# Optimization experiments

Hardware: AMD Instinct MI355X
Metric: run time of the kernel (lower is better)

The kernel has to match this reference:

```python
import jax, jax.numpy as jnp
import numpy as np

COLB = 16            # COL_BLOCK_WIDTH
IN_W = 1024          # input_width; zero_inputs=0 so input_locations = arange(IN_W)
OUT_W = 512          # output_width
DEPTH = 8            # network_depth
IN_L = 4             # butterfly_in_depth
OUT_L = 4            # butterfly_out_depth
ACT = 8              # activations_per_block
BLOCKS = 64          # blocks_per_layer -> num_inputs = 1024 per module
CURV = 1.0
GROW = BLOCKS * ACT  # 512 new rows per module
TOTAL = IN_W + DEPTH * GROW  # 5120
BATCH = 4096


def setup_inputs() -> dict:
    key = jax.random.key(0)
    k1, k2, k3 = jax.random.split(key, 3)
    input_data = jax.random.normal(k1, (IN_W, BATCH), dtype=jnp.float32)
    scales = jnp.full((IN_W,), 0.05, dtype=jnp.float32)
    # angles uniform in (-pi, pi), shape [depth, in_layers+out_layers, num_inputs/2]
    angles = (jax.random.uniform(k2, (DEPTH, IN_L + OUT_L, BLOCKS * COLB // 2)) * 2.0 - 1.0) * np.pi
    angles = angles.astype(jnp.float32)
    biases = jax.random.normal(k3, (DEPTH, GROW), dtype=jnp.float32) * 0.05
    # per-module indices_in = randperm(total_width_so_far)[:num_inputs]
    rng = np.random.RandomState(0)
    tw = IN_W
    idxs = []
    for _ in range(DEPTH):
        idxs.append(rng.permutation(tw)[: BLOCKS * COLB].astype(np.int32))
        tw += GROW
    indices_in = jnp.asarray(np.stack(idxs))  # [depth, 1024]
    return {"input_data": input_data, "scales": scales, "angles": angles,
            "biases": biases, "indices_in": indices_in}


def _rotate(x, ang, stride):
    # x: [W, B]; pair row i (with (i//stride)%2==0) with row i+stride inside 16-blocks
    W, B = x.shape
    xr = x.reshape(W // (2 * stride), 2, stride, B)
    a = ang.reshape(W // (2 * stride), stride)[:, :, None]
    c, s = jnp.cos(a), jnp.sin(a)
    lo, hi = xr[:, 0], xr[:, 1]              # [W/2s, s, B]
    nlo = c * lo + s * hi
    nhi = -s * lo + c * hi
    return jnp.stack([nlo, nhi], axis=1).reshape(W, B)


def _butterfly_module(data, ang, bias, idx, idx_out):
    W = BLOCKS * COLB
    x = data[idx]                             # gather [1024, B]
    for l in range(IN_L):
        x = _rotate(x, ang[l], 2 ** (l % 4))
    xb = x.reshape(BLOCKS, COLB, -1)
    pre = xb[:, :ACT, :] + bias.reshape(BLOCKS, ACT)[:, :, None]
    # curvature (smoothed-ReLU) activation
    act = 0.5 * (pre + jnp.sqrt(pre * pre + CURV * CURV))
    xb = xb.at[:, :ACT, :].set(act)
    x = xb.reshape(W, -1)
    for l in range(OUT_L):
        x = _rotate(x, ang[IN_L + l], 2 ** ((IN_L + l) % 4))
    data = data.at[idx].set(x)                # scatter working set back
    data = data.at[idx_out: idx_out + GROW].set(act.reshape(GROW, -1))
    return data


def reference(input_data, scales, angles, biases, indices_in):
    B = input_data.shape[1]
    data = jnp.zeros((TOTAL, B), dtype=input_data.dtype)
    data = data.at[:IN_W].set(scales[:, None] * input_data)
    for i in range(DEPTH):
        data = _butterfly_module(data, angles[i], biases[i], indices_in[i], IN_W + GROW * i)
    return data[TOTAL - OUT_W:]
```

## Files before the change

### kernel.cpp

```cpp
#include <hip/hip_runtime.h>
#include <math.h>

#define N_INW     1024
#define N_DEPTH   8
#define N_GROW    512
#define N_BATCH   4096
#define N_THREADS 64
#define N_LAYERS  64

typedef __attribute__((ext_vector_type(2))) float F2;
typedef decltype(__builtin_amdgcn_cvt_pkrtz(0.f, 0.f)) H2;

__global__ void precompute_kernel(const float* __restrict__ angles,
                                  const int*   __restrict__ indices,
                                  _Float16* __restrict__ csh,
                                  int*   __restrict__ addrs) {
    int i = blockIdx.x * blockDim.x + threadIdx.x;
    if (i < N_LAYERS * 512) {
        int g = i >> 9, p = i & 511, blk = p >> 3, j = p & 7;
        float a = angles[i];
        _Float16* base = csh + g * 1024 + blk * 16;
        base[j]     = (_Float16)cosf(a);
        base[8 + j] = (_Float16)sinf(a);
    }
    if (i < N_DEPTH * N_INW) {
        int v = indices[i];
        addrs[i] = (v + (v >> 4)) << 2;
    }
}

#define ADDR(r) ((((r) + ((r) >> 4))) << 2)

#define LD2(A) ({ H2 _h = *(const H2*)(L + (A));                               \
                  F2 _v; _v.x = (float)_h.x; _v.y = (float)_h.y; _v; })
#define ST2(A, V) do { F2 _w = (V);                                            \
    *(H2*)(L + (A)) = __builtin_amdgcn_cvt_pkrtz(_w.x, _w.y); } while (0)

#define PKU(x, y) __builtin_bit_cast(unsigned int,                             \
                      __builtin_amdgcn_cvt_pkrtz((x), (y)))

#define UNPK(Q, FA, FB) do {                                                   \
    H2 _h0 = __builtin_bit_cast(H2, (Q).x), _h1 = __builtin_bit_cast(H2, (Q).y),\
       _h2 = __builtin_bit_cast(H2, (Q).z), _h3 = __builtin_bit_cast(H2, (Q).w);\
    FA.x = (float)_h0.x; FA.y = (float)_h0.y; FA.z = (float)_h1.x;             \
    FA.w = (float)_h1.y; FB.x = (float)_h2.x; FB.y = (float)_h2.y;             \
    FB.z = (float)_h3.x; FB.w = (float)_h3.y; } while (0)

#define DECL_SET(P)                                                            \
    uint4 P##c0, P##s0, P##c1, P##s1, P##c2, P##s2, P##c3, P##s3,              \
          P##c4, P##s4, P##c5, P##s5, P##c6, P##s6, P##c7, P##s7;              \
    int4  P##i0, P##i1, P##i2, P##i3;                                          \
    float4 P##bA, P##bB;

#define SYN1(P, K, ANB) do {                                                   \
    const float4* _p = (const float4*)((ANB) + (K)*512 + (blk << 3));          \
    float4 _u = _p[0], _v = _p[1];                                             \
    float _c0,_c1,_c2,_c3,_c4,_c5,_c6,_c7,_t0,_t1,_t2,_t3,_t4,_t5,_t6,_t7;     \
    __sincosf(_u.x,&_t0,&_c0); __sincosf(_u.y,&_t1,&_c1);                      \
    __sincosf(_u.z,&_t2,&_c2); __sincosf(_u.w,&_t3,&_c3);                      \
    __sincosf(_v.x,&_t4,&_c4); __sincosf(_v.y,&_t5,&_c5);                      \
    __sincosf(_v.z,&_t6,&_c6); __sincosf(_v.w,&_t7,&_c7);                      \
    P##c##K = make_uint4(PKU(_c0,_c1),PKU(_c2,_c3),PKU(_c4,_c5),PKU(_c6,_c7)); \
    P##s##K = make_uint4(PKU(_t0,_t1),PKU(_t2,_t3),PKU(_t4,_t5),PKU(_t6,_t7)); \
  } while (0)

#define LOADCS1(P, K, CSN, ANB) do { if (USE_TABLE) {                          \
    const char* _b = (CSN) + (blk << 5) + (K)*2048;                            \
    P##c##K = *(const uint4*)(_b); P##s##K = *(const uint4*)(_b + 16);         \
  } else { SYN1(P, K, ANB); } } while (0)

#define LOADCS8(P, CSN, ANB) do {                                              \
    LOADCS1(P,0,CSN,ANB); LOADCS1(P,1,CSN,ANB); LOADCS1(P,2,CSN,ANB);          \
    LOADCS1(P,3,CSN,ANB); LOADCS1(P,4,CSN,ANB); LOADCS1(P,5,CSN,ANB);          \
    LOADCS1(P,6,CSN,ANB); LOADCS1(P,7,CSN,ANB); } while (0)
#define LOADCS4(P, CSN, ANB) do {                                              \
    LOADCS1(P,0,CSN,ANB); LOADCS1(P,1,CSN,ANB); LOADCS1(P,2,CSN,ANB);          \
    LOADCS1(P,3,CSN,ANB); } while (0)

#define TR(v) (((v) + ((v) >> 4)) << 2)
#define LOAD_AB(P, ATN, INB, BIN) do { if (USE_TABLE) {                        \
    const int4* _ip = (const int4*)((ATN) + (blk << 4));                       \
    P##i0=_ip[0]; P##i1=_ip[1]; P##i2=_ip[2]; P##i3=_ip[3];                    \
  } else {                                                                     \
    const int4* _ip = (const int4*)((INB) + (blk << 4));                       \
    int4 _v0=_ip[0], _v1=_ip[1], _v2=_ip[2], _v3=_ip[3];                       \
    P##i0.x=TR(_v0.x); P##i0.y=TR(_v0.y); P##i0.z=TR(_v0.z); P##i0.w=TR(_v0.w);\
    P##i1.x=TR(_v1.x); P##i1.y=TR(_v1.y); P##i1.z=TR(_v1.z); P##i1.w=TR(_v1.w);\
    P##i2.x=TR(_v2.x); P##i2.y=TR(_v2.y); P##i2.z=TR(_v2.z); P##i2.w=TR(_v2.w);\
    P##i3.x=TR(_v3.x); P##i3.y=TR(_v3.y); P##i3.z=TR(_v3.z); P##i3.w=TR(_v3.w);\
  }                                                                            \
  const float4* _bp = (const float4*)((BIN) + (blk << 3));                     \
  P##bA = _bp[0]; P##bB = _bp[1]; } while (0)

#define ROTP(LO, HI, CC, SS) do { F2 _l = LO, _h = HI;                         \
    LO = CC * _l + SS * _h; HI = CC * _h - SS * _l; } while (0)

#define ROTS1(CA,CB,SA,SB) do {                                                \
    ROTP(x0,x1,CA.x,SA.x);  ROTP(x2,x3,CA.y,SA.y);                             \
    ROTP(x4,x5,CA.z,SA.z);  ROTP(x6,x7,CA.w,SA.w);                             \
    ROTP(x8,x9,CB.x,SB.x);  ROTP(x10,x11,CB.y,SB.y);                           \
    ROTP(x12,x13,CB.z,SB.z);ROTP(x14,x15,CB.w,SB.w); } while (0)
#define ROTS2(CA,CB,SA,SB) do {                                                \
    ROTP(x0,x2,CA.x,SA.x);  ROTP(x1,x3,CA.y,SA.y);                             \
    ROTP(x4,x6,CA.z,SA.z);  ROTP(x5,x7,CA.w,SA.w);                             \
    ROTP(x8,x10,CB.x,SB.x); ROTP(x9,x11,CB.y,SB.y);                            \
    ROTP(x12,x14,CB.z,SB.z);ROTP(x13,x15,CB.w,SB.w); } while (0)
#define ROTS4(CA,CB,SA,SB) do {                                                \
    ROTP(x0,x4,CA.x,SA.x);  ROTP(x1,x5,CA.y,SA.y);                             \
    ROTP(x2,x6,CA.z,SA.z);  ROTP(x3,x7,CA.w,SA.w);                             \
    ROTP(x8,x12,CB.x,SB.x); ROTP(x9,x13,CB.y,SB.y);                            \
    ROTP(x10,x14,CB.z,SB.z);ROTP(x11,x15,CB.w,SB.w); } while (0)
#define ROTS8(CA,CB,SA,SB) do {                                                \
    ROTP(x0,x8,CA.x,SA.x);  ROTP(x1,x9,CA.y,SA.y);                             \
    ROTP(x2,x10,CA.z,SA.z); ROTP(x3,x11,CA.w,SA.w);                            \
    ROTP(x4,x12,CB.x,SB.x); ROTP(x5,x13,CB.y,SB.y);                            \
    ROTP(x6,x14,CB.z,SB.z); ROTP(x7,x15,CB.w,SB.w); } while (0)

#define ROTL(P, K, ROTM) do { float4 _CA,_CB,_SA,_SB;                          \
    UNPK(P##c##K, _CA, _CB); UNPK(P##s##K, _SA, _SB);                          \
    ROTM(_CA,_CB,_SA,_SB); } while (0)

#define ACT1(X, BB) do { F2 _p = (X) + (BB);                                   \
    F2 _t = _p * _p + 1.0f;                                                    \
    F2 _r; _r.x = __builtin_amdgcn_sqrtf(_t.x);                                \
    _r.y = __builtin_amdgcn_sqrtf(_t.y);                                       \
    X = 0.5f * (_p + _r); } while (0)

#define FENCE() __builtin_amdgcn_sched_barrier(0)

#define PROC_MOD(P, N, CSN, ANN, ATN, INB, BIN, M, FULL) do {                  \
  const int a0=P##i0.x, a1=P##i0.y, a2=P##i0.z, a3=P##i0.w,                    \
            a4=P##i1.x, a5=P##i1.y, a6=P##i1.z, a7=P##i1.w,                    \
            a8=P##i2.x, a9=P##i2.y, a10=P##i2.z, a11=P##i2.w,                  \
            a12=P##i3.x, a13=P##i3.y, a14=P##i3.z, a15=P##i3.w;                \
  F2 x0=LD2(a0), x1=LD2(a1), x2=LD2(a2), x3=LD2(a3),                           \
     x4=LD2(a4), x5=LD2(a5), x6=LD2(a6), x7=LD2(a7),                           \
     x8=LD2(a8), x9=LD2(a9), x10=LD2(a10), x11=LD2(a11),                       \
     x12=LD2(a12), x13=LD2(a13), x14=LD2(a14), x15=LD2(a15);                   \
  if (FULL) { LOADCS8(N, CSN, ANN); } else { LOADCS4(N, CSN, ANN); }           \
  FENCE();                                                                     \
                     \
  ROTL(P,0,ROTS1); ROTL(P,1,ROTS2); ROTL(P,2,ROTS4); ROTL(P,3,ROTS8);          \
  ACT1(x0,P##bA.x); ACT1(x1,P##bA.y); ACT1(x2,P##bA.z); ACT1(x3,P##bA.w);      \
  ACT1(x4,P##bB.x); ACT1(x5,P##bB.y); ACT1(x6,P##bB.z); ACT1(x7,P##bB.w);      \
  const int _ab = ADDR(N_INW + (M)*N_GROW + (blk << 3));                       \
  ST2(_ab+ 0,x0); ST2(_ab+ 4,x1); ST2(_ab+ 8,x2); ST2(_ab+12,x3);              \
  ST2(_ab+16,x4); ST2(_ab+20,x5); ST2(_ab+24,x6); ST2(_ab+28,x7);              \
  LOAD_AB(N, ATN, INB, BIN);                                                   \
  FENCE();                                                                     \
  ROTL(P,4,ROTS1); ROTL(P,5,ROTS2); ROTL(P,6,ROTS4); ROTL(P,7,ROTS8);          \
  ST2(a0,x0);  ST2(a1,x1);  ST2(a2,x2);  ST2(a3,x3);                           \
  ST2(a4,x4);  ST2(a5,x5);  ST2(a6,x6);  ST2(a7,x7);                           \
  ST2(a8,x8);  ST2(a9,x9);  ST2(a10,x10); ST2(a11,x11);                        \
  ST2(a12,x12); ST2(a13,x13); ST2(a14,x14); ST2(a15,x15);                      \
} while (0)

template <bool USE_TABLE>
__global__ __launch_bounds__(N_THREADS, 2)
void butterfly_fused_kernel(const float* __restrict__ input,
                            const float* __restrict__ scales,
                            const float* __restrict__ biases,
                            const int*   __restrict__ indices,
                            const char*  __restrict__ cs_tab,
                            const int*   __restrict__ addr_tab,
                            const float* __restrict__ angles,
                            float* __restrict__ out) {
    extern __shared__ float ldsbuf[];
    char* L = (char*)ldsbuf;
    const int blk = threadIdx.x;
    const int b   = blockIdx.x;
    const int cg  = (((b & 7) * 256) + (b >> 3)) * 2;

    DECL_SET(A) DECL_SET(B)

    LOADCS8(A, cs_tab, angles);
    LOAD_AB(A, addr_tab, indices, biases);

#pragma unroll
    for (int k = 0; k < 16; ++k) {
        const int r = (k << 6) + blk;
        F2 v = *(const F2*)(input + (size_t)r * N_BATCH + cg);
        ST2(ADDR(r), scales[r] * v);
    }

    const char*  csn = cs_tab + 16384;
    const float* ann = angles + 4096;
    const int*   atn = addr_tab + N_INW;
    const int*   inb = indices + N_INW;
    const float* bin = biases + N_GROW;

#pragma unroll 1
    for (int t = 0; t < 3; ++t) {
        const int m = 2 * t;
        PROC_MOD(A, B, csn, ann, atn, inb, bin, m, 1);
        csn += 16384; ann += 4096; atn += N_INW; inb += N_INW; bin += N_GROW;
        PROC_MOD(B, A, csn, ann, atn, inb, bin, m + 1, 1);
        csn += 16384; ann += 4096; atn += N_INW; inb += N_INW; bin += N_GROW;
    }
    PROC_MOD(A, B, csn, ann, atn, inb, bin, 6, 0);

    {
        const int a0=Bi0.x, a1=Bi0.y, a2=Bi0.z, a3=Bi0.w,
                  a4=Bi1.x, a5=Bi1.y, a6=Bi1.z, a7=Bi1.w;
        F2 x0=LD2(a0), x1=LD2(a1), x2=LD2(a2), x3=LD2(a3),
           x4=LD2(a4), x5=LD2(a5), x6=LD2(a6), x7=LD2(a7);
        F2 x8=LD2(Bi2.x), x9=LD2(Bi2.y), x10=LD2(Bi2.z), x11=LD2(Bi2.w),
           x12=LD2(Bi3.x), x13=LD2(Bi3.y), x14=LD2(Bi3.z), x15=LD2(Bi3.w);
        FENCE();
        ROTL(B,0,ROTS1); ROTL(B,1,ROTS2); ROTL(B,2,ROTS4); ROTL(B,3,ROTS8);
        ACT1(x0,BbA.x); ACT1(x1,BbA.y); ACT1(x2,BbA.z); ACT1(x3,BbA.w);
        ACT1(x4,BbB.x); ACT1(x5,BbB.y); ACT1(x6,BbB.z); ACT1(x7,BbB.w);
        *(F2*)(out + (size_t)((blk<<3)+0)*N_BATCH + cg) = x0;
        *(F2*)(out + (size_t)((blk<<3)+1)*N_BATCH + cg) = x1;
        *(F2*)(out + (size_t)((blk<<3)+2)*N_BATCH + cg) = x2;
        *(F2*)(out + (size_t)((blk<<3)+3)*N_BATCH + cg) = x3;
        *(F2*)(out + (size_t)((blk<<3)+4)*N_BATCH + cg) = x4;
        *(F2*)(out + (size_t)((blk<<3)+5)*N_BATCH + cg) = x5;
        *(F2*)(out + (size_t)((blk<<3)+6)*N_BATCH + cg) = x6;
        *(F2*)(out + (size_t)((blk<<3)+7)*N_BATCH + cg) = x7;
    }
}

extern "C" void kernel_launch(void* const* d_in, const int* in_sizes, int n_in,
                              void* d_out, int out_size, void* d_ws, size_t ws_size,
                              hipStream_t stream) {
    const float* input   = (const float*)d_in[0];
    const float* scales  = (const float*)d_in[1];
    const float* angles  = (const float*)d_in[2];
    const float* biases  = (const float*)d_in[3];
    const int*   indices = (const int*)d_in[4];
    float* out = (float*)d_out;

    const size_t cs_bytes  = (size_t)N_LAYERS * 2048;
    const size_t adr_bytes = (size_t)N_DEPTH * N_INW * sizeof(int);
    const size_t lds_bytes = (size_t)4608 * 4 + 288 * 4;
    const int grid = N_BATCH / 2;

    if (ws_size >= cs_bytes + adr_bytes) {
        _Float16* csh = (_Float16*)d_ws;
        int* addrs = (int*)((char*)d_ws + cs_bytes);
        precompute_kernel<<<(N_LAYERS * 512 + 255) / 256, 256, 0, stream>>>(
            angles, indices, csh, addrs);
        butterfly_fused_kernel<true><<<grid, N_THREADS, lds_bytes, stream>>>(
            input, scales, biases, indices, (const char*)csh, addrs, angles, out);
    } else {
        butterfly_fused_kernel<false><<<grid, N_THREADS, lds_bytes, stream>>>(
            input, scales, biases, indices, nullptr, nullptr, angles, out);
    }
}
```

Baseline: 100.5 us.

## Run butterfly rotations in packed fp16 and give each block two column-pair slabs

Rotations now run directly on packed half2 values, using broadcast cos/sin halves, instead of unpacking to fp32 and repacking. This removes many conversion instructions per layer, though the rotation arithmetic is now done in fp16 rather than fp32. The activation still runs in fp32 on each element. Blocks grow to 128 threads, where two wavefronts each own their own LDS slab and column pair, and the grid is halved. This amortises per-block setup but may reduce occupancy because each block needs more LDS.

```diff
diff --git a/kernel.cpp b/kernel.cpp
--- a/kernel.cpp
+++ b/kernel.cpp
@@ -5,11 +5,12 @@
 #define N_DEPTH   8
 #define N_GROW    512
 #define N_BATCH   4096
-#define N_THREADS 64
+#define N_THREADS 128
 #define N_LAYERS  64
-
-typedef __attribute__((ext_vector_type(2))) float F2;
-typedef decltype(__builtin_amdgcn_cvt_pkrtz(0.f, 0.f)) H2;
+#define SLAB_B    19584
+
+typedef __attribute__((ext_vector_type(2))) float    F2;
+typedef __attribute__((ext_vector_type(2))) _Float16 h2;
 
 __global__ void precompute_kernel(const float* __restrict__ angles,
                                   const int*   __restrict__ indices,
@@ -31,20 +32,20 @@
 
 #define ADDR(r) ((((r) + ((r) >> 4))) << 2)
 
-#define LD2(A) ({ H2 _h = *(const H2*)(L + (A));                               \
-                  F2 _v; _v.x = (float)_h.x; _v.y = (float)_h.y; _v; })
-#define ST2(A, V) do { F2 _w = (V);                                            \
-    *(H2*)(L + (A)) = __builtin_amdgcn_cvt_pkrtz(_w.x, _w.y); } while (0)
+#define LDH(A)    __builtin_bit_cast(h2, *(const unsigned*)(L + (A)))
+#define STH(A, V) do { *(unsigned*)(L + (A)) =                                 \
+                       __builtin_bit_cast(unsigned, (V)); } while (0)
 
 #define PKU(x, y) __builtin_bit_cast(unsigned int,                             \
                       __builtin_amdgcn_cvt_pkrtz((x), (y)))
 
-#define UNPK(Q, FA, FB) do {                                                   \
-    H2 _h0 = __builtin_bit_cast(H2, (Q).x), _h1 = __builtin_bit_cast(H2, (Q).y),\
-       _h2 = __builtin_bit_cast(H2, (Q).z), _h3 = __builtin_bit_cast(H2, (Q).w);\
-    FA.x = (float)_h0.x; FA.y = (float)_h0.y; FA.z = (float)_h1.x;             \
-    FA.w = (float)_h1.y; FB.x = (float)_h2.x; FB.y = (float)_h2.y;             \
-    FB.z = (float)_h3.x; FB.w = (float)_h3.y; } while (0)
+#define BCL(U) ({ h2 _t = __builtin_bit_cast(h2, (unsigned)(U));               \
+                  h2 _r; _r.x = _t.x; _r.y = _t.x; _r; })
+#define BCH(U) ({ h2 _t = __builtin_bit_cast(h2, (unsigned)(U));               \
+                  h2 _r; _r.x = _t.y; _r.y = _t.y; _r; })
+
+#define ROTPH(LO, HI, CC, SS) do { h2 _l = LO, _h = HI, _c = CC, _s = SS;      \
+    LO = _c * _l + _s * _h; HI = _c * _h - _s * _l; } while (0)
 
 #define DECL_SET(P)                                                            \
     uint4 P##c0, P##s0, P##c1, P##s1, P##c2, P##s2, P##c3, P##s3,              \
@@ -92,39 +93,38 @@
   const float4* _bp = (const float4*)((BIN) + (blk << 3));                     \
   P##bA = _bp[0]; P##bB = _bp[1]; } while (0)
 
-#define ROTP(LO, HI, CC, SS) do { F2 _l = LO, _h = HI;                         \
-    LO = CC * _l + SS * _h; HI = CC * _h - SS * _l; } while (0)
-
-#define ROTS1(CA,CB,SA,SB) do {                                                \
-    ROTP(x0,x1,CA.x,SA.x);  ROTP(x2,x3,CA.y,SA.y);                             \
-    ROTP(x4,x5,CA.z,SA.z);  ROTP(x6,x7,CA.w,SA.w);                             \
-    ROTP(x8,x9,CB.x,SB.x);  ROTP(x10,x11,CB.y,SB.y);                           \
-    ROTP(x12,x13,CB.z,SB.z);ROTP(x14,x15,CB.w,SB.w); } while (0)
-#define ROTS2(CA,CB,SA,SB) do {                                                \
-    ROTP(x0,x2,CA.x,SA.x);  ROTP(x1,x3,CA.y,SA.y);                             \
-    ROTP(x4,x6,CA.z,SA.z);  ROTP(x5,x7,CA.w,SA.w);                             \
-    ROTP(x8,x10,CB.x,SB.x); ROTP(x9,x11,CB.y,SB.y);                            \
-    ROTP(x12,x14,CB.z,SB.z);ROTP(x13,x15,CB.w,SB.w); } while (0)
-#define ROTS4(CA,CB,SA,SB) do {                                                \
-    ROTP(x0,x4,CA.x,SA.x);  ROTP(x1,x5,CA.y,SA.y);                             \
-    ROTP(x2,x6,CA.z,SA.z);  ROTP(x3,x7,CA.w,SA.w);                             \
-    ROTP(x8,x12,CB.x,SB.x); ROTP(x9,x13,CB.y,SB.y);                            \
-    ROTP(x10,x14,CB.z,SB.z);ROTP(x11,x15,CB.w,SB.w); } while (0)
-#define ROTS8(CA,CB,SA,SB) do {                                                \
-    ROTP(x0,x8,CA.x,SA.x);  ROTP(x1,x9,CA.y,SA.y);                             \
-    ROTP(x2,x10,CA.z,SA.z); ROTP(x3,x11,CA.w,SA.w);                            \
-    ROTP(x4,x12,CB.x,SB.x); ROTP(x5,x13,CB.y,SB.y);                            \
-    ROTP(x6,x14,CB.z,SB.z); ROTP(x7,x15,CB.w,SB.w); } while (0)
-
-#define ROTL(P, K, ROTM) do { float4 _CA,_CB,_SA,_SB;                          \
-    UNPK(P##c##K, _CA, _CB); UNPK(P##s##K, _SA, _SB);                          \
-    ROTM(_CA,_CB,_SA,_SB); } while (0)
-
-#define ACT1(X, BB) do { F2 _p = (X) + (BB);                                   \
-    F2 _t = _p * _p + 1.0f;                                                    \
-    F2 _r; _r.x = __builtin_amdgcn_sqrtf(_t.x);                                \
-    _r.y = __builtin_amdgcn_sqrtf(_t.y);                                       \
-    X = 0.5f * (_p + _r); } while (0)
+#define HROTS1(C,S) do {                                                       \
+    ROTPH(x0,x1,  BCL(C.x),BCL(S.x)); ROTPH(x2,x3,  BCH(C.x),BCH(S.x));        \
+    ROTPH(x4,x5,  BCL(C.y),BCL(S.y)); ROTPH(x6,x7,  BCH(C.y),BCH(S.y));        \
+    ROTPH(x8,x9,  BCL(C.z),BCL(S.z)); ROTPH(x10,x11,BCH(C.z),BCH(S.z));        \
+    ROTPH(x12,x13,BCL(C.w),BCL(S.w)); ROTPH(x14,x15,BCH(C.w),BCH(S.w));        \
+  } while (0)
+#define HROTS2(C,S) do {                                                       \
+    ROTPH(x0,x2,  BCL(C.x),BCL(S.x)); ROTPH(x1,x3,  BCH(C.x),BCH(S.x));        \
+    ROTPH(x4,x6,  BCL(C.y),BCL(S.y)); ROTPH(x5,x7,  BCH(C.y),BCH(S.y));        \
+    ROTPH(x8,x10, BCL(C.z),BCL(S.z)); ROTPH(x9,x11, BCH(C.z),BCH(S.z));        \
+    ROTPH(x12,x14,BCL(C.w),BCL(S.w)); ROTPH(x13,x15,BCH(C.w),BCH(S.w));        \
+  } while (0)
+#define HROTS4(C,S) do {                                                       \
+    ROTPH(x0,x4,  BCL(C.x),BCL(S.x)); ROTPH(x1,x5,  BCH(C.x),BCH(S.x));        \
+    ROTPH(x2,x6,  BCL(C.y),BCL(S.y)); ROTPH(x3,x7,  BCH(C.y),BCH(S.y));        \
+    ROTPH(x8,x12, BCL(C.z),BCL(S.z)); ROTPH(x9,x13, BCH(C.z),BCH(S.z));        \
+    ROTPH(x10,x14,BCL(C.w),BCL(S.w)); ROTPH(x11,x15,BCH(C.w),BCH(S.w));        \
+  } while (0)
+#define HROTS8(C,S) do {                                                       \
+    ROTPH(x0,x8,  BCL(C.x),BCL(S.x)); ROTPH(x1,x9,  BCH(C.x),BCH(S.x));        \
+    ROTPH(x2,x10, BCL(C.y),BCL(S.y)); ROTPH(x3,x11, BCH(C.y),BCH(S.y));        \
+    ROTPH(x4,x12, BCL(C.z),BCL(S.z)); ROTPH(x5,x13, BCH(C.z),BCH(S.z));        \
+    ROTPH(x6,x14, BCL(C.w),BCL(S.w)); ROTPH(x7,x15, BCH(C.w),BCH(S.w));        \
+  } while (0)
+
+#define HROT(P, K, M) M(P##c##K, P##s##K)
+
+#define ACTH(X, BF) do {                                                       \
+    float _lo = (float)(X).x + (BF), _hi = (float)(X).y + (BF);                \
+    _lo = 0.5f * (_lo + __builtin_amdgcn_sqrtf(_lo * _lo + 1.0f));             \
+    _hi = 0.5f * (_hi + __builtin_amdgcn_sqrtf(_hi * _hi + 1.0f));             \
+    X = __builtin_bit_cast(h2, PKU(_lo, _hi)); } while (0)
 
 #define FENCE() __builtin_amdgcn_sched_barrier(0)
 
@@ -133,26 +133,25 @@
             a4=P##i1.x, a5=P##i1.y, a6=P##i1.z, a7=P##i1.w,                    \
             a8=P##i2.x, a9=P##i2.y, a10=P##i2.z, a11=P##i2.w,                  \
             a12=P##i3.x, a13=P##i3.y, a14=P##i3.z, a15=P##i3.w;                \
-  F2 x0=LD2(a0), x1=LD2(a1), x2=LD2(a2), x3=LD2(a3),                           \
-     x4=LD2(a4), x5=LD2(a5), x6=LD2(a6), x7=LD2(a7),                           \
-     x8=LD2(a8), x9=LD2(a9), x10=LD2(a10), x11=LD2(a11),                       \
-     x12=LD2(a12), x13=LD2(a13), x14=LD2(a14), x15=LD2(a15);                   \
+  h2 x0=LDH(a0), x1=LDH(a1), x2=LDH(a2), x3=LDH(a3),                           \
+     x4=LDH(a4), x5=LDH(a5), x6=LDH(a6), x7=LDH(a7),                           \
+     x8=LDH(a8), x9=LDH(a9), x10=LDH(a10), x11=LDH(a11),                       \
+     x12=LDH(a12), x13=LDH(a13), x14=LDH(a14), x15=LDH(a15);                   \
   if (FULL) { LOADCS8(N, CSN, ANN); } else { LOADCS4(N, CSN, ANN); }           \
   FENCE();                                                                     \
-                     \
-  ROTL(P,0,ROTS1); ROTL(P,1,ROTS2); ROTL(P,2,ROTS4); ROTL(P,3,ROTS8);          \
-  ACT1(x0,P##bA.x); ACT1(x1,P##bA.y); ACT1(x2,P##bA.z); ACT1(x3,P##bA.w);      \
-  ACT1(x4,P##bB.x); ACT1(x5,P##bB.y); ACT1(x6,P##bB.z); ACT1(x7,P##bB.w);      \
+  HROT(P,0,HROTS1); HROT(P,1,HROTS2); HROT(P,2,HROTS4); HROT(P,3,HROTS8);      \
+  ACTH(x0,P##bA.x); ACTH(x1,P##bA.y); ACTH(x2,P##bA.z); ACTH(x3,P##bA.w);      \
+  ACTH(x4,P##bB.x); ACTH(x5,P##bB.y); ACTH(x6,P##bB.z); ACTH(x7,P##bB.w);      \
   const int _ab = ADDR(N_INW + (M)*N_GROW + (blk << 3));                       \
-  ST2(_ab+ 0,x0); ST2(_ab+ 4,x1); ST2(_ab+ 8,x2); ST2(_ab+12,x3);              \
-  ST2(_ab+16,x4); ST2(_ab+20,x5); ST2(_ab+24,x6); ST2(_ab+28,x7);              \
+  STH(_ab+ 0,x0); STH(_ab+ 4,x1); STH(_ab+ 8,x2); STH(_ab+12,x3);              \
+  STH(_ab+16,x4); STH(_ab+20,x5); STH(_ab+24,x6); STH(_ab+28,x7);              \
   LOAD_AB(N, ATN, INB, BIN);                                                   \
   FENCE();                                                                     \
-  ROTL(P,4,ROTS1); ROTL(P,5,ROTS2); ROTL(P,6,ROTS4); ROTL(P,7,ROTS8);          \
-  ST2(a0,x0);  ST2(a1,x1);  ST2(a2,x2);  ST2(a3,x3);                           \
-  ST2(a4,x4);  ST2(a5,x5);  ST2(a6,x6);  ST2(a7,x7);                           \
-  ST2(a8,x8);  ST2(a9,x9);  ST2(a10,x10); ST2(a11,x11);                        \
-  ST2(a12,x12); ST2(a13,x13); ST2(a14,x14); ST2(a15,x15);                      \
+  HROT(P,4,HROTS1); HROT(P,5,HROTS2); HROT(P,6,HROTS4); HROT(P,7,HROTS8);      \
+  STH(a0,x0);  STH(a1,x1);  STH(a2,x2);  STH(a3,x3);                           \
+  STH(a4,x4);  STH(a5,x5);  STH(a6,x6);  STH(a7,x7);                           \
+  STH(a8,x8);  STH(a9,x9);  STH(a10,x10); STH(a11,x11);                        \
+  STH(a12,x12); STH(a13,x13); STH(a14,x14); STH(a15,x15);                      \
 } while (0)
 
 template <bool USE_TABLE>
@@ -166,10 +165,12 @@
                             const float* __restrict__ angles,
                             float* __restrict__ out) {
     extern __shared__ float ldsbuf[];
-    char* L = (char*)ldsbuf;
-    const int blk = threadIdx.x;
+    const int t   = threadIdx.x;
+    const int blk = t & 63;
+    const int cp  = t >> 6;
+    char* L = (char*)ldsbuf + cp * SLAB_B;
     const int b   = blockIdx.x;
-    const int cg  = (((b & 7) * 256) + (b >> 3)) * 2;
+    const int cg  = ((((b & 7) * 128) + (b >> 3)) << 2) + (cp << 1);
 
     DECL_SET(A) DECL_SET(B)
 
@@ -180,7 +181,7 @@
     for (int k = 0; k < 16; ++k) {
         const int r = (k << 6) + blk;
         F2 v = *(const F2*)(input + (size_t)r * N_BATCH + cg);
-        ST2(ADDR(r), scales[r] * v);
+        STH(ADDR(r), __builtin_bit_cast(h2, PKU(scales[r] * v.x, scales[r] * v.y)));
     }
 
     const char*  csn = cs_tab + 16384;
@@ -190,8 +191,8 @@
     const float* bin = biases + N_GROW;
 
 #pragma unroll 1
-    for (int t = 0; t < 3; ++t) {
-        const int m = 2 * t;
+    for (int tt = 0; tt < 3; ++tt) {
+        const int m = 2 * tt;
         PROC_MOD(A, B, csn, ann, atn, inb, bin, m, 1);
         csn += 16384; ann += 4096; atn += N_INW; inb += N_INW; bin += N_GROW;
         PROC_MOD(B, A, csn, ann, atn, inb, bin, m + 1, 1);
@@ -200,24 +201,19 @@
     PROC_MOD(A, B, csn, ann, atn, inb, bin, 6, 0);
 
     {
-        const int a0=Bi0.x, a1=Bi0.y, a2=Bi0.z, a3=Bi0.w,
-                  a4=Bi1.x, a5=Bi1.y, a6=Bi1.z, a7=Bi1.w;
-        F2 x0=LD2(a0), x1=LD2(a1), x2=LD2(a2), x3=LD2(a3),
-           x4=LD2(a4), x5=LD2(a5), x6=LD2(a6), x7=LD2(a7);
-        F2 x8=LD2(Bi2.x), x9=LD2(Bi2.y), x10=LD2(Bi2.z), x11=LD2(Bi2.w),
-           x12=LD2(Bi3.x), x13=LD2(Bi3.y), x14=LD2(Bi3.z), x15=LD2(Bi3.w);
+        h2 x0=LDH(Bi0.x), x1=LDH(Bi0.y), x2=LDH(Bi0.z), x3=LDH(Bi0.w),
+           x4=LDH(Bi1.x), x5=LDH(Bi1.y), x6=LDH(Bi1.z), x7=LDH(Bi1.w),
+           x8=LDH(Bi2.x), x9=LDH(Bi2.y), x10=LDH(Bi2.z), x11=LDH(Bi2.w),
+           x12=LDH(Bi3.x), x13=LDH(Bi3.y), x14=LDH(Bi3.z), x15=LDH(Bi3.w);
         FENCE();
-        ROTL(B,0,ROTS1); ROTL(B,1,ROTS2); ROTL(B,2,ROTS4); ROTL(B,3,ROTS8);
-        ACT1(x0,BbA.x); ACT1(x1,BbA.y); ACT1(x2,BbA.z); ACT1(x3,BbA.w);
-        ACT1(x4,BbB.x); ACT1(x5,BbB.y); ACT1(x6,BbB.z); ACT1(x7,BbB.w);
-        *(F2*)(out + (size_t)((blk<<3)+0)*N_BATCH + cg) = x0;
-        *(F2*)(out + (size_t)((blk<<3)+1)*N_BATCH + cg) = x1;
-        *(F2*)(out + (size_t)((blk<<3)+2)*N_BATCH + cg) = x2;
-        *(F2*)(out + (size_t)((blk<<3)+3)*N_BATCH + cg) = x3;
-        *(F2*)(out + (size_t)((blk<<3)+4)*N_BATCH + cg) = x4;
-        *(F2*)(out + (size_t)((blk<<3)+5)*N_BATCH + cg) = x5;
-        *(F2*)(out + (size_t)((blk<<3)+6)*N_BATCH + cg) = x6;
-        *(F2*)(out + (size_t)((blk<<3)+7)*N_BATCH + cg) = x7;
+        HROT(B,0,HROTS1); HROT(B,1,HROTS2); HROT(B,2,HROTS4); HROT(B,3,HROTS8);
+        ACTH(x0,BbA.x); ACTH(x1,BbA.y); ACTH(x2,BbA.z); ACTH(x3,BbA.w);
+        ACTH(x4,BbB.x); ACTH(x5,BbB.y); ACTH(x6,BbB.z); ACTH(x7,BbB.w);
+#define OUTW(J, X) do { F2 _o; _o.x = (float)(X).x; _o.y = (float)(X).y;       \
+        *(F2*)(out + (size_t)((blk<<3)+(J))*N_BATCH + cg) = _o; } while (0)
+        OUTW(0,x0); OUTW(1,x1); OUTW(2,x2); OUTW(3,x3);
+        OUTW(4,x4); OUTW(5,x5); OUTW(6,x6); OUTW(7,x7);
+#undef OUTW
     }
 }
 
@@ -233,8 +229,8 @@
 
     const size_t cs_bytes  = (size_t)N_LAYERS * 2048;
     const size_t adr_bytes = (size_t)N_DEPTH * N_INW * sizeof(int);
-    const size_t lds_bytes = (size_t)4608 * 4 + 288 * 4;
-    const int grid = N_BATCH / 2;
+    const size_t lds_bytes = (size_t)2 * SLAB_B;
+    const int grid = N_BATCH / 4;
 
     if (ws_size >= cs_bytes + adr_bytes) {
         _Float16* csh = (_Float16*)d_ws;
```

After: 98.33 us. 1.02x faster.
